# Optimization experiments

Measured on AMD Instinct MI355X. Metric: run time of the kernel, lower is better.

## Reference

```python
import jax, jax.numpy as jnp
import numpy as np

EMB = 4096
HEADS = 32
SCALE = 4
D = EMB // HEADS          # qkv_dim = 128
HKV = HEADS // SCALE      # 8 kv heads
B, S = 2, 2048


def setup_inputs() -> dict:
    key = jax.random.key(0)
    ks = jax.random.split(key, 7)
    std = 0.02
    return {
        "x": jax.random.normal(ks[0], (B, S, EMB), jnp.float32),
        "Wq": jax.random.normal(ks[1], (EMB, D, HEADS), jnp.float32) * std,
        "bq": jnp.zeros((D, HEADS), jnp.float32),
        "Wk": jax.random.normal(ks[2], (EMB, D, HKV), jnp.float32) * std,
        "bk": jnp.zeros((D, HKV), jnp.float32),
        "Wv": jax.random.normal(ks[3], (EMB, D, HKV), jnp.float32) * std,
        "bv": jnp.zeros((D, HKV), jnp.float32),
    }


def reference(x, Wq, bq, Wk, bk, Wv, bv):
    # DenseGeneral projections: (B,S,E) -> (B,S,D,H)
    q = jnp.einsum("bse,edh->bsdh", x, Wq) + bq          # [B,S,D,H]
    k = jnp.einsum("bse,edh->bsdh", x, Wk) + bk          # [B,S,D,Hkv]
    v = jnp.einsum("bse,edh->bsdh", x, Wv) + bv          # [B,S,D,Hkv]
    # repeat kv heads (each kv head duplicated SCALE times, matching jnp.repeat)
    k = jnp.repeat(k, SCALE, axis=-1)                    # [B,S,D,H]
    v = jnp.repeat(v, SCALE, axis=-1)                    # [B,S,D,H]
    # NOTE: as written in the source, attention contracts the HEAD axis per
    # token: scores are (qkv_dim x qkv_dim) per (b, s) position.
    scores = jnp.einsum("bsdh,bseh->bsde", q, k) / np.float32(np.sqrt(D))
    attn = jax.nn.softmax(scores, axis=-1)               # [B,S,D,D]
    out = jnp.einsum("bsde,bseh->bsdh", attn, v)         # [B,S,D,H]
    return out.reshape(x.shape[:-1] + (EMB,))
```

## Files before the change

kernel.cpp:

```cpp
#include <hip/hip_runtime.h>
#include <cstdint>

typedef unsigned short ushort_t;
typedef __bf16 bf16x8 __attribute__((ext_vector_type(8)));
typedef float f32x4 __attribute__((ext_vector_type(4)));

__device__ __forceinline__ unsigned short f2bf(float f) {
  unsigned u = __builtin_bit_cast(unsigned, f);
  u += 0x7FFFu + ((u >> 16) & 1u);
  return (unsigned short)(u >> 16);
}
__device__ __forceinline__ float bflo(unsigned u) {
  return __builtin_bit_cast(float, u << 16);
}
__device__ __forceinline__ float bfhi(unsigned u) {
  return __builtin_bit_cast(float, u & 0xFFFF0000u);
}
__device__ __forceinline__ void gld16(const void* g, void* l) {
  auto* gp = reinterpret_cast<const __attribute__((address_space(1))) unsigned*>(
      reinterpret_cast<uintptr_t>(g));
  auto* lp = reinterpret_cast<__attribute__((address_space(3))) unsigned*>(
      reinterpret_cast<uintptr_t>(l));
  __builtin_amdgcn_global_load_lds(gp, lp, 16, 0, 0);
}

__global__ __launch_bounds__(256) void prep_all(
    const float* __restrict__ x, const float* __restrict__ Wq,
    const float* __restrict__ Wk, const float* __restrict__ Wv,
    const float* __restrict__ bq, const float* __restrict__ bk,
    const float* __restrict__ bv, ushort_t* __restrict__ Ax,
    ushort_t* __restrict__ Wt, float* __restrict__ bias) {
  __shared__ ushort_t red[64][65];
  const int b = blockIdx.x;
  const int tid = threadIdx.x;
  if (b < 3072) {
    const int ntile = b % 48, ktile = b / 48;
    const int n0 = ntile * 64, k0 = ktile * 64;
    if (ntile < 16) {
      for (int i = tid; i < 64 * 64; i += 256) {
        const int kk = i >> 6, nn = i & 63;
        const float4 w = *reinterpret_cast<const float4*>(
            Wq + (size_t)(k0 + kk) * 4096 + (size_t)(n0 + nn) * 4);
        red[kk][nn] = f2bf(w.x + w.y + w.z + w.w);
      }
    } else {
      const float* W = (ntile < 32) ? Wk : Wv;
      const int nb = (ntile < 32) ? (n0 - 1024) : (n0 - 2048);
      for (int i = tid; i < 64 * 64; i += 256) {
        const int kk = i >> 6, nn = i & 63;
        red[kk][nn] = f2bf(W[(size_t)(k0 + kk) * 1024 + nb + nn]);
      }
    }
    __syncthreads();
    for (int i = tid; i < 64 * 64; i += 256) {
      const int kk = i & 63, nn = i >> 6;
      Wt[(size_t)(n0 + nn) * 4096 + k0 + kk] = red[kk][nn];
    }
  } else if (b < 11264) {
    const size_t i = ((size_t)(b - 3072) * 256 + tid) * 8;
    const float4 a = *reinterpret_cast<const float4*>(x + i);
    const float4 c = *reinterpret_cast<const float4*>(x + i + 4);
    union { ushort_t u[8]; uint4 v; } pk;
    pk.u[0] = f2bf(a.x); pk.u[1] = f2bf(a.y); pk.u[2] = f2bf(a.z); pk.u[3] = f2bf(a.w);
    pk.u[4] = f2bf(c.x); pk.u[5] = f2bf(c.y); pk.u[6] = f2bf(c.z); pk.u[7] = f2bf(c.w);
    *reinterpret_cast<uint4*>(Ax + i) = pk.v;
  } else {
    const int n = (b - 11264) * 256 + tid;
    float v;
    if (n < 1024) {
      const float4 w = *reinterpret_cast<const float4*>(bq + (size_t)n * 4);
      v = w.x + w.y + w.z + w.w;
    } else if (n < 2048) {
      v = bk[n - 1024];
    } else {
      v = bv[n - 2048];
    }
    bias[n] = v;
  }
}

#define WAITV0() asm volatile("s_waitcnt vmcnt(0)" ::: "memory")
#define BARRIER()                         \
  do {                                    \
    __builtin_amdgcn_s_barrier();         \
    asm volatile("" ::: "memory");        \
    __builtin_amdgcn_sched_barrier(0);    \
  } while (0)

__global__ __launch_bounds__(512, 2) void gemm_qkv(const ushort_t* __restrict__ A,
                                                   const ushort_t* __restrict__ Bt,
                                                   const float* __restrict__ bias,
                                                   ushort_t* __restrict__ C) {
  __shared__ ushort_t As[2][256 * 64];
  __shared__ ushort_t Bs[2][192 * 64];
  const int tid = threadIdx.x;
  const int lane = tid & 63, wave = tid >> 6;

  const int id = blockIdx.x;
  const int wg = (id & 7) * 32 + (id >> 3);
  const int M0 = (wg >> 4) * 256, N0 = (wg & 15) * 192;

  const int rik = lane >> 3;
  const int gch = (lane & 7) ^ rik;
  const ushort_t* aG = A + (size_t)(M0 + wave * 32 + rik) * 4096 + gch * 8;
  const ushort_t* bG = Bt + (size_t)(N0 + wave * 24 + rik) * 4096 + gch * 8;

  const int wm = wave >> 2, wn = wave & 3;
  const int quad = lane >> 4, l15 = lane & 15;

  f32x4 acc[8][3];
  const f32x4 z = {0.f, 0.f, 0.f, 0.f};
#pragma unroll
  for (int mi = 0; mi < 8; ++mi)
#pragma unroll
    for (int ni = 0; ni < 3; ++ni) acc[mi][ni] = z;

  auto stage = [&](int bb, int kt) {
    const int ko = kt * 64;
#pragma unroll
    for (int q = 0; q < 4; ++q)
      gld16(aG + ko + (size_t)q * (8 * 4096), &As[bb][(wave * 4 + q) * 512]);
#pragma unroll
    for (int q = 0; q < 3; ++q)
      gld16(bG + ko + (size_t)q * (8 * 4096), &Bs[bb][(wave * 3 + q) * 512]);
  };

  stage(0, 0);
  WAITV0();
  BARRIER();

  for (int kt = 0; kt < 64; ++kt) {
    const int bb = kt & 1;
    if (kt < 63) stage(bb ^ 1, kt + 1);
#pragma unroll
    for (int ks = 0; ks < 2; ++ks) {
      bf16x8 af[8], bfr[3];
#pragma unroll
      for (int mi = 0; mi < 8; ++mi) {
        const int row = wm * 128 + mi * 16 + l15;
        const int ch = ((ks * 4 + quad) ^ (row & 7)) * 8;
        af[mi] = *reinterpret_cast<const bf16x8*>(&As[bb][row * 64 + ch]);
      }
#pragma unroll
      for (int ni = 0; ni < 3; ++ni) {
        const int row = wn * 48 + ni * 16 + l15;
        const int ch = ((ks * 4 + quad) ^ (row & 7)) * 8;
        bfr[ni] = *reinterpret_cast<const bf16x8*>(&Bs[bb][row * 64 + ch]);
      }
      __builtin_amdgcn_s_setprio(1);
#pragma unroll
      for (int mi = 0; mi < 8; ++mi)
#pragma unroll
        for (int ni = 0; ni < 3; ++ni)
          acc[mi][ni] =
              __builtin_amdgcn_mfma_f32_16x16x32_bf16(af[mi], bfr[ni], acc[mi][ni], 0, 0, 0);
      __builtin_amdgcn_s_setprio(0);
    }
    WAITV0();
    BARRIER();
  }

#pragma unroll
  for (int ni = 0; ni < 3; ++ni) {
    const int cc = N0 + wn * 48 + ni * 16 + l15;
    const float bn = bias[cc];
#pragma unroll
    for (int mi = 0; mi < 8; ++mi) {
      const int r0 = M0 + wm * 128 + mi * 16 + quad * 4;
#pragma unroll
      for (int r = 0; r < 4; ++r)
        C[(size_t)(r0 + r) * 3072 + cc] = f2bf(acc[mi][ni][r] + bn);
    }
  }
}

__global__ __launch_bounds__(256, 4) void attn_tok(const ushort_t* __restrict__ C,
                                                   float* __restrict__ out) {
  __shared__ uint4 kv4[4][256];
  const int tid = threadIdx.x;
  const int lane = tid & 63, wv = tid >> 6;
  const int t = blockIdx.x * 4 + wv;
  const ushort_t* Crow = C + (size_t)t * 3072;

  const uint4* src = reinterpret_cast<const uint4*>(Crow + 1024);
#pragma unroll
  for (int r = 0; r < 4; ++r) kv4[wv][r * 64 + lane] = src[r * 64 + lane];
  __syncthreads();

  const uint4 q01 = *reinterpret_cast<const uint4*>(Crow + lane * 16);
  const uint4 q23 = *reinterpret_cast<const uint4*>(Crow + lane * 16 + 8);
  float qa[8], qb[8];
  qa[0] = bflo(q01.x); qa[1] = bfhi(q01.x); qa[2] = bflo(q01.y); qa[3] = bfhi(q01.y);
  qa[4] = bflo(q01.z); qa[5] = bfhi(q01.z); qa[6] = bflo(q01.w); qa[7] = bfhi(q01.w);
  qb[0] = bflo(q23.x); qb[1] = bfhi(q23.x); qb[2] = bflo(q23.y); qb[3] = bfhi(q23.y);
  qb[4] = bflo(q23.z); qb[5] = bfhi(q23.z); qb[6] = bflo(q23.w); qb[7] = bfhi(q23.w);

  const uint4* kvw = kv4[wv];
  const float sc = 0.08838834764831845f;
  float oa[8], ob[8];
#pragma unroll
  for (int j = 0; j < 8; ++j) { oa[j] = 0.f; ob[j] = 0.f; }
  float l0 = 0.f, l1 = 0.f;

#pragma unroll 2
  for (int e = 0; e < 128; ++e) {
    const uint4 kr = kvw[e];
    float kf[8];
    kf[0] = bflo(kr.x); kf[1] = bfhi(kr.x); kf[2] = bflo(kr.y); kf[3] = bfhi(kr.y);
    kf[4] = bflo(kr.z); kf[5] = bfhi(kr.z); kf[6] = bflo(kr.w); kf[7] = bfhi(kr.w);
    float s0 = 0.f, s1 = 0.f;
#pragma unroll
    for (int j = 0; j < 8; ++j) { s0 += qa[j] * kf[j]; s1 += qb[j] * kf[j]; }
    const float p0 = __expf(s0 * sc);
    const float p1 = __expf(s1 * sc);
    l0 += p0; l1 += p1;
    const uint4 vr = kvw[128 + e];
    float vf[8];
    vf[0] = bflo(vr.x); vf[1] = bfhi(vr.x); vf[2] = bflo(vr.y); vf[3] = bfhi(vr.y);
    vf[4] = bflo(vr.z); vf[5] = bfhi(vr.z); vf[6] = bflo(vr.w); vf[7] = bfhi(vr.w);
#pragma unroll
    for (int j = 0; j < 8; ++j) { oa[j] += p0 * vf[j]; ob[j] += p1 * vf[j]; }
  }

  const float i0 = 1.f / l0, i1 = 1.f / l1;
  float4* dst = reinterpret_cast<float4*>(out + (size_t)t * 4096 + (size_t)lane * 64);
#pragma unroll
  for (int j = 0; j < 8; ++j) {
    const float w = oa[j] * i0;
    dst[j] = make_float4(w, w, w, w);
  }
#pragma unroll
  for (int j = 0; j < 8; ++j) {
    const float w = ob[j] * i1;
    dst[8 + j] = make_float4(w, w, w, w);
  }
}

extern "C" void kernel_launch(void* const* d_in, const int* in_sizes, int n_in,
                              void* d_out, int out_size, void* d_ws, size_t ws_size,
                              hipStream_t stream) {
  const float* x  = (const float*)d_in[0];
  const float* Wq = (const float*)d_in[1];
  const float* bq = (const float*)d_in[2];
  const float* Wk = (const float*)d_in[3];
  const float* bk = (const float*)d_in[4];
  const float* Wv = (const float*)d_in[5];
  const float* bv = (const float*)d_in[6];
  float* out = (float*)d_out;

  ushort_t* Ax = (ushort_t*)d_out;
  ushort_t* Wt = Ax + (size_t)4096 * 4096;
  float* bias = (float*)(Wt + (size_t)3072 * 4096);
  ushort_t* Cmat = (ushort_t*)d_ws;

  prep_all<<<dim3(11276), 256, 0, stream>>>(x, Wq, Wk, Wv, bq, bk, bv, Ax, Wt, bias);
  gemm_qkv<<<dim3(256), 512, 0, stream>>>(Ax, Wt, bias, Cmat);
  attn_tok<<<dim3(1024), 256, 0, stream>>>(Cmat, out);
}
```

Baseline: 347.9 us.

## Split K across wave pairs in QKV GEMM with LDS reduction of partial sums

Reorganizes the 8 waves of the QKV GEMM so that pairs of waves split each 64-wide K tile in half. Each wave now computes a larger 128x96 output subtile, which raises fragment reuse per LDS read. The two K-halves are then summed through LDS scratch in a two-pass epilogue before the bias is added and bf16 is stored. This doubles accumulator registers per wave (48 f32x4) and adds an epilogue reduction with extra barriers, so there is a risk of register spilling or lower occupancy under launch_bounds(512,2).

```diff
diff --git a/kernel.cpp b/kernel.cpp
--- a/kernel.cpp
+++ b/kernel.cpp
@@ -91,8 +91,9 @@
                                                    const ushort_t* __restrict__ Bt,
                                                    const float* __restrict__ bias,
                                                    ushort_t* __restrict__ C) {
-  __shared__ ushort_t As[2][256 * 64];
-  __shared__ ushort_t Bs[2][192 * 64];
+  __shared__ char smem[114688];
+  ushort_t* AsBuf = reinterpret_cast<ushort_t*>(smem);
+  ushort_t* BsBuf = reinterpret_cast<ushort_t*>(smem + 65536);
   const int tid = threadIdx.x;
   const int lane = tid & 63, wave = tid >> 6;
 
@@ -105,24 +106,31 @@
   const ushort_t* aG = A + (size_t)(M0 + wave * 32 + rik) * 4096 + gch * 8;
   const ushort_t* bG = Bt + (size_t)(N0 + wave * 24 + rik) * 4096 + gch * 8;
 
-  const int wm = wave >> 2, wn = wave & 3;
+  const int kh = wave & 1, wq = wave >> 1;
+  const int wm = wq >> 1, wn = wq & 1;
   const int quad = lane >> 4, l15 = lane & 15;
 
-  f32x4 acc[8][3];
+  const int ch = ((kh * 4 + quad) ^ (l15 & 7)) * 16;
+  const int abase = (wm * 128 + l15) * 128 + ch;
+  const int bbase = (wn * 96 + l15) * 128 + ch;
+
+  f32x4 acc[8][6];
   const f32x4 z = {0.f, 0.f, 0.f, 0.f};
 #pragma unroll
   for (int mi = 0; mi < 8; ++mi)
 #pragma unroll
-    for (int ni = 0; ni < 3; ++ni) acc[mi][ni] = z;
+    for (int ni = 0; ni < 6; ++ni) acc[mi][ni] = z;
 
   auto stage = [&](int bb, int kt) {
     const int ko = kt * 64;
+    ushort_t* asb = AsBuf + bb * 16384;
+    ushort_t* bsb = BsBuf + bb * 12288;
 #pragma unroll
     for (int q = 0; q < 4; ++q)
-      gld16(aG + ko + (size_t)q * (8 * 4096), &As[bb][(wave * 4 + q) * 512]);
+      gld16(aG + ko + (size_t)q * (8 * 4096), asb + (wave * 4 + q) * 512);
 #pragma unroll
     for (int q = 0; q < 3; ++q)
-      gld16(bG + ko + (size_t)q * (8 * 4096), &Bs[bb][(wave * 3 + q) * 512]);
+      gld16(bG + ko + (size_t)q * (8 * 4096), bsb + (wave * 3 + q) * 512);
   };
 
   stage(0, 0);
@@ -132,44 +140,56 @@
   for (int kt = 0; kt < 64; ++kt) {
     const int bb = kt & 1;
     if (kt < 63) stage(bb ^ 1, kt + 1);
-#pragma unroll
-    for (int ks = 0; ks < 2; ++ks) {
-      bf16x8 af[8], bfr[3];
-#pragma unroll
-      for (int mi = 0; mi < 8; ++mi) {
-        const int row = wm * 128 + mi * 16 + l15;
-        const int ch = ((ks * 4 + quad) ^ (row & 7)) * 8;
-        af[mi] = *reinterpret_cast<const bf16x8*>(&As[bb][row * 64 + ch]);
-      }
-#pragma unroll
-      for (int ni = 0; ni < 3; ++ni) {
-        const int row = wn * 48 + ni * 16 + l15;
-        const int ch = ((ks * 4 + quad) ^ (row & 7)) * 8;
-        bfr[ni] = *reinterpret_cast<const bf16x8*>(&Bs[bb][row * 64 + ch]);
-      }
+    const char* ab = reinterpret_cast<const char*>(AsBuf + bb * 16384);
+    const char* bbp = reinterpret_cast<const char*>(BsBuf + bb * 12288);
+    bf16x8 af[8];
+#pragma unroll
+    for (int mi = 0; mi < 8; ++mi)
+      af[mi] = *reinterpret_cast<const bf16x8*>(ab + abase + mi * 2048);
+#pragma unroll
+    for (int ni = 0; ni < 6; ++ni) {
+      const bf16x8 bf = *reinterpret_cast<const bf16x8*>(bbp + bbase + ni * 2048);
       __builtin_amdgcn_s_setprio(1);
 #pragma unroll
       for (int mi = 0; mi < 8; ++mi)
-#pragma unroll
-        for (int ni = 0; ni < 3; ++ni)
-          acc[mi][ni] =
-              __builtin_amdgcn_mfma_f32_16x16x32_bf16(af[mi], bfr[ni], acc[mi][ni], 0, 0, 0);
+        acc[mi][ni] =
+            __builtin_amdgcn_mfma_f32_16x16x32_bf16(af[mi], bf, acc[mi][ni], 0, 0, 0);
       __builtin_amdgcn_s_setprio(0);
     }
     WAITV0();
     BARRIER();
   }
 
-#pragma unroll
-  for (int ni = 0; ni < 3; ++ni) {
-    const int cc = N0 + wn * 48 + ni * 16 + l15;
-    const float bn = bias[cc];
-#pragma unroll
-    for (int mi = 0; mi < 8; ++mi) {
-      const int r0 = M0 + wm * 128 + mi * 16 + quad * 4;
-#pragma unroll
-      for (int r = 0; r < 4; ++r)
-        C[(size_t)(r0 + r) * 3072 + cc] = f2bf(acc[mi][ni][r] + bn);
+  float* scr = reinterpret_cast<float*>(smem);
+  const int slot = (wq * 64 + lane) * 97;
+#pragma unroll
+  for (int p = 0; p < 2; ++p) {
+    __syncthreads();
+    if (kh == 1) {
+#pragma unroll
+      for (int mi = 0; mi < 4; ++mi)
+#pragma unroll
+        for (int ni = 0; ni < 6; ++ni)
+#pragma unroll
+          for (int r = 0; r < 4; ++r)
+            scr[slot + (mi * 6 + ni) * 4 + r] = acc[p * 4 + mi][ni][r];
+    }
+    __syncthreads();
+    if (kh == 0) {
+#pragma unroll
+      for (int ni = 0; ni < 6; ++ni) {
+        const int cc = N0 + wn * 96 + ni * 16 + l15;
+        const float bn = bias[cc];
+#pragma unroll
+        for (int mi = 0; mi < 4; ++mi) {
+          const int gmi = p * 4 + mi;
+          const int r0 = M0 + wm * 128 + gmi * 16 + quad * 4;
+#pragma unroll
+          for (int r = 0; r < 4; ++r)
+            C[(size_t)(r0 + r) * 3072 + cc] =
+                f2bf(acc[gmi][ni][r] + scr[slot + (mi * 6 + ni) * 4 + r] + bn);
+        }
+      }
     }
   }
 }
```

Result: no change. 351.6 us (+1.1%).
